# Kernel tuning notes

Hardware: AMD Instinct MI355X
Metric: run time of the kernel (lower is better)

## Reference

```python
import jax, jax.numpy as jnp
import numpy as np

B, N, L = 64, 256, 1024
OUT = L // 2   # ChebConv out_channels = Seq_len / 2
ALPHA = 0.5    # DirGNNConv default alpha


def _glorot(key, shape):
    # PyG ChebConv lins use glorot init
    lim = float(np.sqrt(6.0 / (shape[0] + shape[1])))
    return jax.random.uniform(key, shape, minval=-lim, maxval=lim, dtype=jnp.float32)


def setup_inputs() -> dict:
    key = jax.random.key(0)
    ks = jax.random.split(key, 8)
    x = jax.random.normal(ks[0], (B, N, L), dtype=jnp.float32)
    # dense per-sample adjacency; only used via nonzero() in torch, never enters math (K=1)
    At = jax.random.randint(ks[1], (B, N, N), 0, 2, dtype=jnp.int32)
    W_in = _glorot(ks[2], (L, OUT))
    b_in = jnp.zeros((OUT,), dtype=jnp.float32)
    W_out = _glorot(ks[3], (L, OUT))
    b_out = jnp.zeros((OUT,), dtype=jnp.float32)
    # DirGNNConv root Linear (kaiming-ish uniform; exact init irrelevant for correctness baseline)
    lim = float(1.0 / np.sqrt(L))
    W_root = jax.random.uniform(ks[4], (L, OUT), minval=-lim, maxval=lim, dtype=jnp.float32)
    b_root = jax.random.uniform(ks[5], (OUT,), minval=-lim, maxval=lim, dtype=jnp.float32)
    return {"x": x, "At": At, "W_in": W_in, "b_in": b_in,
            "W_out": W_out, "b_out": b_out, "W_root": W_root, "b_root": b_root}


def reference(x, At, W_in, b_in, W_out, b_out, W_root, b_root):
    # so the batched edge_index built from At.nonzero() never influences the output.
    # DirGNNConv: alpha * conv_out(x) + (1-alpha) * conv_in(x) + root_lin(x).
    xf = x.reshape(B * N, L)                        # [B*N, L]
    y = (ALPHA * (xf @ W_out + b_out)
         + (1.0 - ALPHA) * (xf @ W_in + b_in)
         + (xf @ W_root + b_root))                  # [B*N, OUT]
    return y.reshape(B, N, OUT)
```

## Files before the change

kernel.cpp:

```cpp
#include <hip/hip_runtime.h>
#include <stdint.h>

static constexpr int Mrows = 16384;
static constexpr int Kdim  = 1024;
static constexpr int Ncols = 512;

typedef __attribute__((ext_vector_type(8))) short bf16x8;
typedef __attribute__((ext_vector_type(4))) float f32x4;

__device__ __forceinline__ unsigned short f2bf(float f) {
  unsigned u = __builtin_bit_cast(unsigned, f);
  u += 0x7FFFu + ((u >> 16) & 1u);
  return (unsigned short)(u >> 16);
}
__device__ __forceinline__ unsigned f2bf2(float lo, float hi) {
  unsigned ul = __builtin_bit_cast(unsigned, lo);
  unsigned uh = __builtin_bit_cast(unsigned, hi);
  ul += 0x7FFFu + ((ul >> 16) & 1u);
  uh += 0x7FFFu + ((uh >> 16) & 1u);
  return (ul >> 16) | (uh & 0xFFFF0000u);
}

__device__ __forceinline__ void gl2lds16(const void* g, void* l) {
  __builtin_amdgcn_global_load_lds(
      (const __attribute__((address_space(1))) void*)g,
      (__attribute__((address_space(3))) void*)l, 16, 0, 0);
}

__global__ __launch_bounds__(256) void prep_w(
    const float* __restrict__ Win, const float* __restrict__ Wout,
    const float* __restrict__ Wroot, unsigned short* __restrict__ Wt)
{
  __shared__ unsigned short lds[32 * 36];
  const int t  = threadIdx.x;
  const int b2 = blockIdx.x;
  const int tk0 = (b2 & 31) * 32;
  const int tn0 = (b2 >> 5) * 32;
  {
    const int k  = t >> 3;
    const int nq = (t & 7) * 4;
    const int gi = (tk0 + k) * Ncols + tn0 + nq;
    const float4 wi = *(const float4*)(Win + gi);
    const float4 wo = *(const float4*)(Wout + gi);
    const float4 wr = *(const float4*)(Wroot + gi);
    lds[(nq + 0) * 36 + k] = f2bf(0.5f * (wi.x + wo.x) + wr.x);
    lds[(nq + 1) * 36 + k] = f2bf(0.5f * (wi.y + wo.y) + wr.y);
    lds[(nq + 2) * 36 + k] = f2bf(0.5f * (wi.z + wo.z) + wr.z);
    lds[(nq + 3) * 36 + k] = f2bf(0.5f * (wi.w + wo.w) + wr.w);
  }
  __syncthreads();
  {
    const int n  = t >> 3;
    const int k8 = (t & 7) * 4;
    const ushort4 v = *(const ushort4*)&lds[n * 36 + k8];
    *(ushort4*)(Wt + (size_t)(tn0 + n) * Kdim + tk0 + k8) = v;
  }
}

__global__ __launch_bounds__(256, 2) void gemm_fused(
    const float* __restrict__ x, const unsigned short* __restrict__ Wt,
    const float* __restrict__ b_in, const float* __restrict__ b_out,
    const float* __restrict__ b_root, float* __restrict__ Y)
{
  constexpr int BUF = 128 * 32;
  __shared__ __attribute__((aligned(16))) short As[2 * BUF];
  __shared__ __attribute__((aligned(16))) short Bs[2 * BUF];

  const int bid = blockIdx.x;
  const int m0 = (bid & 127) * 128;
  const int n0 = (bid >> 7) * 128;

  const int t    = threadIdx.x;
  const int lane = t & 63;
  const int w    = t >> 6;
  const int wm   = w >> 1;
  const int wn   = w & 1;
  const int quad = lane >> 4;
  const int lm   = lane & 15;

  const int sr = lane >> 2;
  const int ss = lane & 3;
  const int sc = ss ^ ((sr >> 1) & 3);
  const float* gX          = x  + (size_t)(m0 + w * 32 + sr) * Kdim + sc * 8;
  const unsigned short* gB = Wt + (size_t)(n0 + w * 32 + sr) * Kdim + sc * 8;
  short* const lA  = &As[(w * 32 + sr) * 32 + ss * 8];
  short* const lB0 = &Bs[(w * 32) * 32];
  short* const lB1 = lB0 + 16 * 32;
  const int rowK = 16 * Kdim;

  const int slot = quad ^ ((lm >> 1) & 3);
  const int aoff = (wm * 64 + lm) * 32 + slot * 8;
  const int boff = (wn * 64 + lm) * 32 + slot * 8;

  f32x4 acc[4][4] = {};
  float4 S0, S1, S2, S3, T0, T1, T2, T3;

#define LOADA(P0, P1, P2, P3, IDX) do {                                   \
    const float* gx_ = gX + (IDX) * 32;                                   \
    P0 = *(const float4*)(gx_);                                           \
    P1 = *(const float4*)(gx_ + 4);                                       \
    P2 = *(const float4*)(gx_ + rowK);                                    \
    P3 = *(const float4*)(gx_ + rowK + 4);                                \
  } while (0)

#define PACKA(P0, P1, P2, P3, NXT) do {                                   \
    uint4 pa_, pb_;                                                       \
    pa_.x = f2bf2(P0.x, P0.y); pa_.y = f2bf2(P0.z, P0.w);                 \
    pa_.z = f2bf2(P1.x, P1.y); pa_.w = f2bf2(P1.z, P1.w);                 \
    pb_.x = f2bf2(P2.x, P2.y); pb_.y = f2bf2(P2.z, P2.w);                 \
    pb_.z = f2bf2(P3.x, P3.y); pb_.w = f2bf2(P3.z, P3.w);                 \
    *(uint4*)(lA + (NXT) * BUF)           = pa_;                          \
    *(uint4*)(lA + (NXT) * BUF + 16 * 32) = pb_;                          \
  } while (0)

#define SYNC() do {                                                       \
    asm volatile("s_waitcnt vmcnt(4) lgkmcnt(0)" ::: "memory");           \
    __builtin_amdgcn_s_barrier();                                         \
    __builtin_amdgcn_sched_barrier(0);                                    \
  } while (0)

#define KSTEP(TT, QA0, QA1, QA2, QA3, RA0, RA1, RA2, RA3) do {            \
    const int cur_ = (TT) & 1, nxt_ = cur_ ^ 1;                           \
    gl2lds16(gB + ((TT) + 1) * 32,        lB0 + nxt_ * BUF);              \
    gl2lds16(gB + ((TT) + 1) * 32 + rowK, lB1 + nxt_ * BUF);              \
    __builtin_amdgcn_sched_barrier(0);   \
    bf16x8 af[4], bfr[4];                                                 \
    _Pragma("unroll") for (int i = 0; i < 4; ++i)                         \
      af[i]  = *(const bf16x8*)&As[cur_ * BUF + aoff + i * 16 * 32];      \
    _Pragma("unroll") for (int j = 0; j < 4; ++j)                         \
      bfr[j] = *(const bf16x8*)&Bs[cur_ * BUF + boff + j * 16 * 32];      \
    PACKA(QA0, QA1, QA2, QA3, nxt_);                                      \
    { int ld_ = (TT) + 2; if (ld_ > 31) ld_ = 31;                         \
      LOADA(RA0, RA1, RA2, RA3, ld_); }                                   \
    _Pragma("unroll") for (int i = 0; i < 4; ++i)                         \
      _Pragma("unroll") for (int j = 0; j < 4; ++j)                       \
        acc[i][j] = __builtin_amdgcn_mfma_f32_16x16x32_bf16(              \
            af[i], bfr[j], acc[i][j], 0, 0, 0);                           \
    SYNC();                                                               \
  } while (0)

  LOADA(S0, S1, S2, S3, 0);
  gl2lds16(gB, lB0);
  gl2lds16(gB + rowK, lB1);
  __builtin_amdgcn_sched_barrier(0);
  LOADA(T0, T1, T2, T3, 1);
  PACKA(S0, S1, S2, S3, 0);
  SYNC();

  #pragma unroll 1
  for (int it = 0; it < 30; it += 2) {
    KSTEP(it,     T0, T1, T2, T3, S0, S1, S2, S3);
    KSTEP(it + 1, S0, S1, S2, S3, T0, T1, T2, T3);
  }
  KSTEP(30, T0, T1, T2, T3, S0, S1, S2, S3);

  {
    bf16x8 af[4], bfr[4];
    #pragma unroll
    for (int i = 0; i < 4; ++i) af[i]  = *(const bf16x8*)&As[BUF + aoff + i * 16 * 32];
    #pragma unroll
    for (int j = 0; j < 4; ++j) bfr[j] = *(const bf16x8*)&Bs[BUF + boff + j * 16 * 32];
    #pragma unroll
    for (int i = 0; i < 4; ++i)
      #pragma unroll
      for (int j = 0; j < 4; ++j)
        acc[i][j] = __builtin_amdgcn_mfma_f32_16x16x32_bf16(af[i], bfr[j], acc[i][j], 0, 0, 0);
  }

#undef KSTEP
#undef SYNC
#undef PACKA
#undef LOADA

  #pragma unroll
  for (int j = 0; j < 4; ++j) {
    const int gc = n0 + wn * 64 + j * 16 + lm;
    const float bias = 0.5f * (b_in[gc] + b_out[gc]) + b_root[gc];
    #pragma unroll
    for (int i = 0; i < 4; ++i) {
      const int gr = m0 + wm * 64 + i * 16 + quad * 4;
      float* yp = Y + (size_t)gr * Ncols + gc;
      #pragma unroll
      for (int r = 0; r < 4; ++r)
        yp[(size_t)r * Ncols] = acc[i][j][r] + bias;
    }
  }
}

extern "C" void kernel_launch(void* const* d_in, const int* in_sizes, int n_in,
                              void* d_out, int out_size, void* d_ws, size_t ws_size,
                              hipStream_t stream)
{
  const float* x      = (const float*)d_in[0];
  const float* W_in   = (const float*)d_in[2];
  const float* b_in   = (const float*)d_in[3];
  const float* W_out  = (const float*)d_in[4];
  const float* b_out  = (const float*)d_in[5];
  const float* W_root = (const float*)d_in[6];
  const float* b_root = (const float*)d_in[7];
  float* y = (float*)d_out;

  unsigned short* Wt = (unsigned short*)d_ws;

  prep_w<<<dim3(512), dim3(256), 0, stream>>>(W_in, W_out, W_root, Wt);
  gemm_fused<<<dim3(512), dim3(256), 0, stream>>>(x, Wt, b_in, b_out, b_root, y);
}
```

Measured before the change: 159.0 us.

## Reshape GEMM tiles to 64x256 with XCD-aware block mapping

The block tile changes from 128x128 to 64 rows by 256 columns. Each wave now computes 32x128 outputs with a 2x8 MFMA accumulator grid and loads fewer fp32 x values per K step. Block IDs are remapped so that the two column halves of the same row tile land on the same XCD, meant to let x rows be shared through that XCD's L2. In exchange, each block stages a larger share of the bf16 weight tile into LDS, and the wider per-wave B fragments raise register pressure.

After: 156.9 us. Within noise of the previous version (-1.3%).

```diff
diff --git a/kernel.cpp b/kernel.cpp
--- a/kernel.cpp
+++ b/kernel.cpp
@@ -1,7 +1,6 @@
 #include <hip/hip_runtime.h>
 #include <stdint.h>
 
-static constexpr int Mrows = 16384;
 static constexpr int Kdim  = 1024;
 static constexpr int Ncols = 512;
 
@@ -62,13 +61,18 @@
     const float* __restrict__ b_in, const float* __restrict__ b_out,
     const float* __restrict__ b_root, float* __restrict__ Y)
 {
-  constexpr int BUF = 128 * 32;
-  __shared__ __attribute__((aligned(16))) short As[2 * BUF];
-  __shared__ __attribute__((aligned(16))) short Bs[2 * BUF];
-
-  const int bid = blockIdx.x;
-  const int m0 = (bid & 127) * 128;
-  const int n0 = (bid >> 7) * 128;
+  constexpr int ABUF = 64 * 32;
+  constexpr int BBUF = 256 * 32;
+  __shared__ __attribute__((aligned(16))) short As[2 * ABUF];
+  __shared__ __attribute__((aligned(16))) short Bs[2 * BBUF];
+
+  const int bid  = blockIdx.x;
+  const int xcd  = bid & 7;
+  const int idx  = bid >> 3;
+  const int mt   = xcd * 32 + (idx >> 1);
+  const int half = idx & 1;
+  const int m0   = mt * 64;
+  const int n0   = half * 256;
 
   const int t    = threadIdx.x;
   const int lane = t & 63;
@@ -78,107 +82,111 @@
   const int quad = lane >> 4;
   const int lm   = lane & 15;
 
+  const int arow = w * 16 + (lane >> 2);
+  const int ac   = lane & 3;
+  const float* gX = x + (size_t)(m0 + arow) * Kdim + ac * 8;
+  short* const lA = &As[arow * 32 + (ac ^ ((lane >> 3) & 3)) * 8];
+
   const int sr = lane >> 2;
   const int ss = lane & 3;
   const int sc = ss ^ ((sr >> 1) & 3);
-  const float* gX          = x  + (size_t)(m0 + w * 32 + sr) * Kdim + sc * 8;
-  const unsigned short* gB = Wt + (size_t)(n0 + w * 32 + sr) * Kdim + sc * 8;
-  short* const lA  = &As[(w * 32 + sr) * 32 + ss * 8];
-  short* const lB0 = &Bs[(w * 32) * 32];
-  short* const lB1 = lB0 + 16 * 32;
+  const unsigned short* gB = Wt + (size_t)(n0 + w * 64 + sr) * Kdim + sc * 8;
+  short* const lB = &Bs[(w * 64) * 32];
   const int rowK = 16 * Kdim;
 
   const int slot = quad ^ ((lm >> 1) & 3);
-  const int aoff = (wm * 64 + lm) * 32 + slot * 8;
-  const int boff = (wn * 64 + lm) * 32 + slot * 8;
-
-  f32x4 acc[4][4] = {};
-  float4 S0, S1, S2, S3, T0, T1, T2, T3;
-
-#define LOADA(P0, P1, P2, P3, IDX) do {                                   \
+  const int aoff = (wm * 32 + lm) * 32 + slot * 8;
+  const int boff = (wn * 128 + lm) * 32 + slot * 8;
+
+  f32x4 acc[2][8] = {};
+  float4 S0, S1, T0, T1;
+
+#define LOADX(P0, P1, IDX) do {                                           \
     const float* gx_ = gX + (IDX) * 32;                                   \
     P0 = *(const float4*)(gx_);                                           \
     P1 = *(const float4*)(gx_ + 4);                                       \
-    P2 = *(const float4*)(gx_ + rowK);                                    \
-    P3 = *(const float4*)(gx_ + rowK + 4);                                \
-  } while (0)
-
-#define PACKA(P0, P1, P2, P3, NXT) do {                                   \
-    uint4 pa_, pb_;                                                       \
-    pa_.x = f2bf2(P0.x, P0.y); pa_.y = f2bf2(P0.z, P0.w);                 \
-    pa_.z = f2bf2(P1.x, P1.y); pa_.w = f2bf2(P1.z, P1.w);                 \
-    pb_.x = f2bf2(P2.x, P2.y); pb_.y = f2bf2(P2.z, P2.w);                 \
-    pb_.z = f2bf2(P3.x, P3.y); pb_.w = f2bf2(P3.z, P3.w);                 \
-    *(uint4*)(lA + (NXT) * BUF)           = pa_;                          \
-    *(uint4*)(lA + (NXT) * BUF + 16 * 32) = pb_;                          \
+  } while (0)
+
+#define PACKA(P0, P1, NXT) do {                                           \
+    uint4 pk_;                                                            \
+    pk_.x = f2bf2(P0.x, P0.y); pk_.y = f2bf2(P0.z, P0.w);                 \
+    pk_.z = f2bf2(P1.x, P1.y); pk_.w = f2bf2(P1.z, P1.w);                 \
+    *(uint4*)(lA + (NXT) * ABUF) = pk_;                                   \
+  } while (0)
+
+#define STAGE_B(TT, BUF) do {                                             \
+    gl2lds16(gB + (TT) * 32,            lB + (BUF) * BBUF);               \
+    gl2lds16(gB + (TT) * 32 + rowK,     lB + (BUF) * BBUF + 16 * 32);     \
+    gl2lds16(gB + (TT) * 32 + 2 * rowK, lB + (BUF) * BBUF + 32 * 32);     \
+    gl2lds16(gB + (TT) * 32 + 3 * rowK, lB + (BUF) * BBUF + 48 * 32);     \
   } while (0)
 
 #define SYNC() do {                                                       \
-    asm volatile("s_waitcnt vmcnt(4) lgkmcnt(0)" ::: "memory");           \
+    asm volatile("s_waitcnt vmcnt(2) lgkmcnt(0)" ::: "memory");           \
     __builtin_amdgcn_s_barrier();                                         \
     __builtin_amdgcn_sched_barrier(0);                                    \
   } while (0)
 
-#define KSTEP(TT, QA0, QA1, QA2, QA3, RA0, RA1, RA2, RA3) do {            \
-    const int cur_ = (TT) & 1, nxt_ = cur_ ^ 1;                           \
-    gl2lds16(gB + ((TT) + 1) * 32,        lB0 + nxt_ * BUF);              \
-    gl2lds16(gB + ((TT) + 1) * 32 + rowK, lB1 + nxt_ * BUF);              \
-    __builtin_amdgcn_sched_barrier(0);   \
-    bf16x8 af[4], bfr[4];                                                 \
-    _Pragma("unroll") for (int i = 0; i < 4; ++i)                         \
-      af[i]  = *(const bf16x8*)&As[cur_ * BUF + aoff + i * 16 * 32];      \
-    _Pragma("unroll") for (int j = 0; j < 4; ++j)                         \
-      bfr[j] = *(const bf16x8*)&Bs[cur_ * BUF + boff + j * 16 * 32];      \
-    PACKA(QA0, QA1, QA2, QA3, nxt_);                                      \
+#define KSTEP(TT, PK0, PK1, LD0, LD1) do {                                \
+    const int nxt_ = ((TT) + 1) & 1, cur_ = (TT) & 1;                     \
+    STAGE_B((TT) + 1, nxt_);                                              \
+    __builtin_amdgcn_sched_barrier(0);    \
+    bf16x8 af[2], bfr[8];                                                 \
+    _Pragma("unroll") for (int i = 0; i < 2; ++i)                         \
+      af[i]  = *(const bf16x8*)&As[cur_ * ABUF + aoff + i * 512];         \
+    _Pragma("unroll") for (int j = 0; j < 8; ++j)                         \
+      bfr[j] = *(const bf16x8*)&Bs[cur_ * BBUF + boff + j * 512];         \
+    PACKA(PK0, PK1, nxt_);                                                \
     { int ld_ = (TT) + 2; if (ld_ > 31) ld_ = 31;                         \
-      LOADA(RA0, RA1, RA2, RA3, ld_); }                                   \
-    _Pragma("unroll") for (int i = 0; i < 4; ++i)                         \
-      _Pragma("unroll") for (int j = 0; j < 4; ++j)                       \
+      LOADX(LD0, LD1, ld_); }                                             \
+    _Pragma("unroll") for (int i = 0; i < 2; ++i)                         \
+      _Pragma("unroll") for (int j = 0; j < 8; ++j)                       \
         acc[i][j] = __builtin_amdgcn_mfma_f32_16x16x32_bf16(              \
             af[i], bfr[j], acc[i][j], 0, 0, 0);                           \
     SYNC();                                                               \
   } while (0)
 
-  LOADA(S0, S1, S2, S3, 0);
-  gl2lds16(gB, lB0);
-  gl2lds16(gB + rowK, lB1);
+  LOADX(S0, S1, 0);
   __builtin_amdgcn_sched_barrier(0);
-  LOADA(T0, T1, T2, T3, 1);
-  PACKA(S0, S1, S2, S3, 0);
+  STAGE_B(0, 0);
+  __builtin_amdgcn_sched_barrier(0);
+  LOADX(T0, T1, 1);
+  PACKA(S0, S1, 0);
   SYNC();
 
   #pragma unroll 1
   for (int it = 0; it < 30; it += 2) {
-    KSTEP(it,     T0, T1, T2, T3, S0, S1, S2, S3);
-    KSTEP(it + 1, S0, S1, S2, S3, T0, T1, T2, T3);
-  }
-  KSTEP(30, T0, T1, T2, T3, S0, S1, S2, S3);
+    KSTEP(it,     T0, T1, S0, S1);
+    KSTEP(it + 1, S0, S1, T0, T1);
+  }
+  KSTEP(30, T0, T1, S0, S1);
 
   {
-    bf16x8 af[4], bfr[4];
-    #pragma unroll
-    for (int i = 0; i < 4; ++i) af[i]  = *(const bf16x8*)&As[BUF + aoff + i * 16 * 32];
-    #pragma unroll
-    for (int j = 0; j < 4; ++j) bfr[j] = *(const bf16x8*)&Bs[BUF + boff + j * 16 * 32];
-    #pragma unroll
-    for (int i = 0; i < 4; ++i)
+    bf16x8 af[2], bfr[8];
+    #pragma unroll
+    for (int i = 0; i < 2; ++i) af[i]  = *(const bf16x8*)&As[ABUF + aoff + i * 512];
+    #pragma unroll
+    for (int j = 0; j < 8; ++j) bfr[j] = *(const bf16x8*)&Bs[BBUF + boff + j * 512];
+    #pragma unroll
+    for (int i = 0; i < 2; ++i)
       #pragma unroll
-      for (int j = 0; j < 4; ++j)
+      for (int j = 0; j < 8; ++j)
         acc[i][j] = __builtin_amdgcn_mfma_f32_16x16x32_bf16(af[i], bfr[j], acc[i][j], 0, 0, 0);
   }
 
 #undef KSTEP
 #undef SYNC
+#undef STAGE_B
 #undef PACKA
-#undef LOADA
+#undef LOADX
 
   #pragma unroll
-  for (int j = 0; j < 4; ++j) {
-    const int gc = n0 + wn * 64 + j * 16 + lm;
+  for (int j = 0; j < 8; ++j) {
+    const int gc = n0 + wn * 128 + j * 16 + lm;
     const float bias = 0.5f * (b_in[gc] + b_out[gc]) + b_root[gc];
     #pragma unroll
-    for (int i = 0; i < 4; ++i) {
-      const int gr = m0 + wm * 64 + i * 16 + quad * 4;
+    for (int i = 0; i < 2; ++i) {
+      const int gr = m0 + wm * 32 + i * 16 + quad * 4;
       float* yp = Y + (size_t)gr * Ncols + gc;
       #pragma unroll
       for (int r = 0; r < 4; ++r)
```
